# Performance work log

Hardware: AMD Instinct MI355X
Metric: run time of the kernel (lower is better)

Reference implementation:

```python
import jax, jax.numpy as jnp
import numpy as np


def causal_fft_conv(v, h):
    # v: [B, L, D], h: [L, D]; causal (linear, not circular) conv via zero-padded FFT
    L = v.shape[1]
    n = 2 * L
    Vf = jnp.fft.rfft(v, n=n, axis=1)          # [B, n//2+1, D]
    Hf = jnp.fft.rfft(h, n=n, axis=0)          # [n//2+1, D]
    y = jnp.fft.irfft(Vf * Hf[None], n=n, axis=1)
    return y[:, :L].astype(v.dtype)


def setup_inputs() -> dict:
    key = jax.random.key(0)
    ks = jax.random.split(key, 5)
    B, L, D = 4, 4096, 1024
    scale = 1.0 / np.sqrt(D)
    x = jax.random.normal(ks[0], (B, L, D), dtype=jnp.float32)
    Wu = jax.random.normal(ks[1], (D, D), dtype=jnp.float32) * scale
    Wv = jax.random.normal(ks[2], (D, D), dtype=jnp.float32) * scale
    Wo = jax.random.normal(ks[3], (D, D), dtype=jnp.float32) * scale
    h_filter = jax.random.normal(ks[4], (L, D), dtype=jnp.float32) * 0.02
    bu = jnp.zeros((D,), jnp.float32)
    bv = jnp.zeros((D,), jnp.float32)
    bo = jnp.zeros((D,), jnp.float32)
    return {"x": x, "Wu": Wu, "bu": bu, "Wv": Wv, "bv": bv,
            "h_filter": h_filter, "Wo": Wo, "bo": bo}


def reference(x, Wu, bu, Wv, bv, h_filter, Wo, bo):
    L = x.shape[1]
    u = jnp.einsum('bld,de->ble', x, Wu) + bu
    v = jnp.einsum('bld,de->ble', x, Wv) + bv
    t = jnp.arange(L, dtype=x.dtype)
    decay = jnp.exp(-0.01 * t)[:, None]          # [L, 1]
    h = h_filter * decay                          # [L, D]
    v_conv = causal_fft_conv(v, h)                # [B, L, D]
    y = u * v_conv
    y = jnp.einsum('bld,de->ble', y, Wo) + bo
    return y
```

## Files before the change

kernel.cpp:

```cpp
#include <hip/hip_runtime.h>
#include <hip/hip_bf16.h>
#include <hip/hip_fp16.h>
#include <string.h>

typedef __hip_bfloat16 bf16;
typedef _Float16 f16;
typedef __attribute__((ext_vector_type(8))) short short8;
typedef __attribute__((ext_vector_type(4))) float floatx4;
typedef __attribute__((ext_vector_type(4))) unsigned int uintx4;

#define GLD16(gp, lp) __builtin_amdgcn_global_load_lds( \
    (__attribute__((address_space(1))) void*)(gp),      \
    (__attribute__((address_space(3))) void*)(lp), 16, 0, 0)

__device__ __forceinline__ unsigned short bf16_bits(float f) {
  bf16 h = (bf16)f;
  unsigned short s;
  memcpy(&s, &h, 2);
  return s;
}

__global__ __launch_bounds__(256)
void cvtx_k(const float* __restrict__ x, char* __restrict__ outbase,
            size_t bstride) {
  size_t e = ((size_t)blockIdx.x * 256 + threadIdx.x) * 8;
  int b = (int)(e >> 22);
  size_t i = e & 4194303;
  const floatx4* s = (const floatx4*)(x + e);
  floatx4 a0 = s[0], a1 = s[1];
  union { uintx4 u4; unsigned short us[8]; } w;
  w.us[0] = bf16_bits(a0.x); w.us[1] = bf16_bits(a0.y);
  w.us[2] = bf16_bits(a0.z); w.us[3] = bf16_bits(a0.w);
  w.us[4] = bf16_bits(a1.x); w.us[5] = bf16_bits(a1.y);
  w.us[6] = bf16_bits(a1.z); w.us[7] = bf16_bits(a1.w);
  *(uintx4*)((bf16*)(outbase + (size_t)b * bstride) + i) = w.u4;
}

__global__ __launch_bounds__(256)
void transpose_k(const float* __restrict__ W0, const float* __restrict__ W1,
                 const float* __restrict__ W2, bf16* __restrict__ T0,
                 bf16* __restrict__ T1, bf16* __restrict__ T2) {
  __shared__ bf16 t[64][66];
  const float* S = blockIdx.z == 0 ? W0 : (blockIdx.z == 1 ? W1 : W2);
  bf16* Dst      = blockIdx.z == 0 ? T0 : (blockIdx.z == 1 ? T1 : T2);
  const int tx = threadIdx.x & 63, ty = threadIdx.x >> 6;
  const int kb = blockIdx.y * 64, nb = blockIdx.x * 64;
#pragma unroll
  for (int rr = 0; rr < 16; ++rr) {
    int r = ty * 16 + rr;
    t[r][tx] = (bf16)S[(size_t)(kb + r) * 1024 + nb + tx];
  }
  __syncthreads();
#pragma unroll
  for (int rr = 0; rr < 16; ++rr) {
    int r = ty * 16 + rr;
    Dst[(size_t)(nb + r) * 1024 + kb + tx] = t[tx][r];
  }
}

__global__ __launch_bounds__(256)
void hprep_k(const float* __restrict__ hf, f16* __restrict__ hp) {
  int idx = blockIdx.x * 256 + threadIdx.x;
  int dblk = idx >> 14;
  int rem = idx & 16383;
  int k = rem >> 5, dd = rem & 31;
  int d = dblk * 32 + dd;
  float val = hf[(size_t)k * 1024 + d] * __expf(-0.01f * (float)k);
  hp[idx] = (f16)val;
}

__device__ __forceinline__
void gemm_body(const bf16* __restrict__ A, const bf16* __restrict__ Bt,
               const float* __restrict__ bias, void* __restrict__ Cout,
               int out_mode, int m0, int n0) {
  constexpr int K = 1024;
  __shared__ __align__(16) bf16 As[128 * 32];
  __shared__ __align__(16) bf16 Bs[128 * 32];
  const int tid = threadIdx.x;
  const int lane = tid & 63;
  const int wave = tid >> 6;
  const int wm = wave >> 1, wn = wave & 1;
  const int r = lane & 15, q = lane >> 4;

  floatx4 acc[4][4] = {};

  const int s0 = tid, s1 = 256 + tid;
  const bf16* gA0 = A + (size_t)(m0 + (s0 >> 2)) * K + (s0 & 3) * 8;
  const bf16* gA1 = A + (size_t)(m0 + (s1 >> 2)) * K + (s1 & 3) * 8;
  const bf16* gB0 = Bt + (size_t)(n0 + (s0 >> 2)) * K + (s0 & 3) * 8;
  const bf16* gB1 = Bt + (size_t)(n0 + (s1 >> 2)) * K + (s1 & 3) * 8;
  char* AsB = (char*)As + wave * 1024;
  char* BsB = (char*)Bs + wave * 1024;

  for (int k0 = 0; k0 < K; k0 += 32) {
    GLD16(gA0 + k0, AsB);
    GLD16(gA1 + k0, AsB + 4096);
    GLD16(gB0 + k0, BsB);
    GLD16(gB1 + k0, BsB + 4096);
    __syncthreads();
    short8 af[4], bfr[4];
#pragma unroll
    for (int i = 0; i < 4; ++i)
      af[i] = *(const short8*)&As[(wm * 64 + i * 16 + r) * 32 + q * 8];
#pragma unroll
    for (int i = 0; i < 4; ++i)
      bfr[i] = *(const short8*)&Bs[(wn * 64 + i * 16 + r) * 32 + q * 8];
#pragma unroll
    for (int mi = 0; mi < 4; ++mi)
#pragma unroll
      for (int ni = 0; ni < 4; ++ni)
        acc[mi][ni] = __builtin_amdgcn_mfma_f32_16x16x32_bf16(
            af[mi], bfr[ni], acc[mi][ni], 0, 0, 0);
    __syncthreads();
  }

  const int cb = n0 + wn * 64;
  float bvv[4];
#pragma unroll
  for (int ni = 0; ni < 4; ++ni) bvv[ni] = bias[cb + ni * 16 + r];
#pragma unroll
  for (int mi = 0; mi < 4; ++mi) {
    int rowb = m0 + wm * 64 + mi * 16 + q * 4;
#pragma unroll
    for (int ni = 0; ni < 4; ++ni) {
      int col = cb + ni * 16 + r;
#pragma unroll
      for (int v = 0; v < 4; ++v) {
        float val = acc[mi][ni][v] + bvv[ni];
        size_t off = (size_t)(rowb + v) * 1024 + col;
        if (out_mode == 0)      ((bf16*)Cout)[off] = (bf16)val;
        else if (out_mode == 1) ((f16*)Cout)[off] = (f16)val;
        else                    ((float*)Cout)[off] = val;
      }
    }
  }
}

__global__ __launch_bounds__(256)
void gemm_uv_k(const bf16* __restrict__ A, const bf16* __restrict__ WuT,
               const bf16* __restrict__ WvT, const float* __restrict__ bu,
               const float* __restrict__ bv, bf16* __restrict__ u_out,
               f16* __restrict__ v_out) {
  const int isv = blockIdx.z;
  gemm_body(A, isv ? WvT : WuT, isv ? bv : bu,
            isv ? (void*)v_out : (void*)u_out, isv,
            blockIdx.x * 128, blockIdx.y * 128);
}

__global__ __launch_bounds__(256)
void gemm_o_k(const bf16* __restrict__ A, const bf16* __restrict__ Bt,
              const float* __restrict__ bias, float* __restrict__ C) {
  gemm_body(A, Bt, bias, (void*)C, 2, blockIdx.x * 128, blockIdx.y * 128);
}

__global__ __launch_bounds__(256)
void conv_k(const f16* __restrict__ vg0, const f16* __restrict__ hp,
            bf16* __restrict__ up0) {
  constexpr int KC = 128, D = 1024;
  __shared__ __align__(16) f16 hs[KC * 32];
  __shared__ __align__(16) f16 vs[256 * 32];
  const int tid = threadIdx.x;
  const int dd = tid & 31, tg = tid >> 5;
  const int d0 = blockIdx.x * 32;
  const int t0 = blockIdx.y * 128;
  const int base = tg * 16;
  const f16* vg = vg0 + (size_t)blockIdx.z * 4096 * D;
  bf16* up = up0 + (size_t)blockIdx.z * 4096 * D;

  float acc[16];
#pragma unroll
  for (int i = 0; i < 16; ++i) acc[i] = 0.f;

  const unsigned* vg32 = (const unsigned*)vg;
  unsigned* vs32 = (unsigned*)vs;
  const uintx4* hsrc = (const uintx4*)(hp + (size_t)blockIdx.x * 512 * 32);
  uintx4* hdst = (uintx4*)hs;

  for (int c = 0; c < 4; ++c) {
    const int k0 = c * KC;
    __syncthreads();
    hdst[tid] = hsrc[k0 * 4 + tid];
    hdst[tid + 256] = hsrc[k0 * 4 + tid + 256];
#pragma unroll
    for (int it = 0; it < 16; ++it) {
      int w = it * 256 + tid;
      int to = w >> 4, dp = w & 15;
      int tau = t0 - k0 - 128 + to;
      unsigned val = 0;
      if (tau >= 0) val = vg32[(size_t)tau * (D / 2) + (d0 >> 1) + dp];
      vs32[w] = val;
    }
    __syncthreads();
    float p[16];
#pragma unroll
    for (int i = 0; i < 16; ++i)
      p[i] = (float)vs[(base + i + 128) * 32 + dd];
    for (int kb = 0; kb < KC / 16; ++kb) {
#pragma unroll
      for (int k2 = 0; k2 < 16; ++k2) {
        const int kk = kb * 16 + k2;
        float hk = (float)hs[kk * 32 + dd];
#pragma unroll
        for (int i = 0; i < 16; ++i)
          acc[i] += hk * p[(i - k2) & 15];
        p[(15 - k2) & 15] = (float)vs[(base + 127 - kk) * 32 + dd];
      }
    }
  }

  const size_t rb = (size_t)(t0 + base) * D + d0 + dd;
#pragma unroll
  for (int i = 0; i < 16; ++i) {
    float uv = (float)up[rb + (size_t)i * D];
    up[rb + (size_t)i * D] = (bf16)(uv * acc[i]);
  }
}

extern "C" void kernel_launch(void* const* d_in, const int* in_sizes, int n_in,
                              void* d_out, int out_size, void* d_ws,
                              size_t ws_size, hipStream_t stream) {
  const float* x  = (const float*)d_in[0];
  const float* Wu = (const float*)d_in[1];
  const float* bu = (const float*)d_in[2];
  const float* Wv = (const float*)d_in[3];
  const float* bv = (const float*)d_in[4];
  const float* hf = (const float*)d_in[5];
  const float* Wo = (const float*)d_in[6];
  const float* bo = (const float*)d_in[7];
  char* ws = (char*)d_ws;
  bf16* WuT = (bf16*)(ws);
  bf16* WvT = (bf16*)(ws + 2097152);
  bf16* WoT = (bf16*)(ws + 4194304);
  f16*  hp  = (f16*)(ws + 6291456);

  dim3 tb(256);
  transpose_k<<<dim3(16, 16, 3), tb, 0, stream>>>(Wu, Wv, Wo, WuT, WvT, WoT);
  hprep_k<<<dim3(2048), tb, 0, stream>>>(hf, hp);

  if (ws_size >= 42991616ull) {
    bf16* xb = (bf16*)d_out;
    f16*  vf = (f16*)((char*)d_out + 33554432);
    bf16* u  = (bf16*)(ws + 8388608);
    cvtx_k<<<dim3(8192), tb, 0, stream>>>(x, (char*)d_out, 8388608);
    gemm_uv_k<<<dim3(128, 8, 2), tb, 0, stream>>>(xb, WuT, WvT, bu, bv, u, vf);
    conv_k<<<dim3(32, 32, 4), tb, 0, stream>>>(vf, hp, u);
    gemm_o_k<<<dim3(128, 8), tb, 0, stream>>>(u, WoT, bo, (float*)d_out);
  } else {
    bf16* u_b = (bf16*)(ws + 8388608);
    cvtx_k<<<dim3(8192), tb, 0, stream>>>(x, (char*)d_out, 16777216);
    for (int b = 0; b < 4; ++b) {
      char* quarter = (char*)d_out + (size_t)b * 16777216;
      bf16* xb = (bf16*)quarter;
      f16*  vb = (f16*)(quarter + 8388608);
      float* outb = (float*)d_out + (size_t)b * 4194304;
      gemm_uv_k<<<dim3(32, 8, 2), tb, 0, stream>>>(xb, WuT, WvT, bu, bv,
                                                   u_b, vb);
      conv_k<<<dim3(32, 32, 1), tb, 0, stream>>>(vb, hp, u_b);
      gemm_o_k<<<dim3(32, 8), tb, 0, stream>>>(u_b, WoT, bo, outb);
    }
  }
}
```

Before: 516.3 us.

## Use packed half2 FMA in causal conv with per-chunk fp16 accumulation

The direct-convolution kernel now has each thread process two adjacent channels as __half2, using packed __hfma2 instead of scalar fp32 FMAs. Partial sums accumulate in fp16 over each 64-tap chunk and are then folded into fp32 accumulators. Tiles now cover 64 channels with 128-bit loads, the filter prep layout changes to match, and the u-gating epilogue works on packed bf16 pairs. This targets ALU throughput in the convolution, at the cost of lower accumulation precision.

```diff
diff --git a/kernel.cpp b/kernel.cpp
--- a/kernel.cpp
+++ b/kernel.cpp
@@ -18,6 +18,11 @@
   unsigned short s;
   memcpy(&s, &h, 2);
   return s;
+}
+__device__ __forceinline__ __half2 u2h2(unsigned u) {
+  __half2 h;
+  memcpy(&h, &u, 4);
+  return h;
 }
 
 __global__ __launch_bounds__(256)
@@ -61,10 +66,10 @@
 __global__ __launch_bounds__(256)
 void hprep_k(const float* __restrict__ hf, f16* __restrict__ hp) {
   int idx = blockIdx.x * 256 + threadIdx.x;
-  int dblk = idx >> 14;
-  int rem = idx & 16383;
-  int k = rem >> 5, dd = rem & 31;
-  int d = dblk * 32 + dd;
+  int dblk = idx >> 15;
+  int rem = idx & 32767;
+  int k = rem >> 6, dd = rem & 63;
+  int d = dblk * 64 + dd;
   float val = hf[(size_t)k * 1024 + d] * __expf(-0.01f * (float)k);
   hp[idx] = (f16)val;
 }
@@ -156,63 +161,81 @@
 __global__ __launch_bounds__(256)
 void conv_k(const f16* __restrict__ vg0, const f16* __restrict__ hp,
             bf16* __restrict__ up0) {
-  constexpr int KC = 128, D = 1024;
-  __shared__ __align__(16) f16 hs[KC * 32];
-  __shared__ __align__(16) f16 vs[256 * 32];
+  constexpr int CC = 64, TT = 128, D = 1024;
+  __shared__ __align__(16) unsigned vs2[(TT + CC) * 32];
+  __shared__ __align__(16) unsigned hs2[CC * 32];
   const int tid = threadIdx.x;
-  const int dd = tid & 31, tg = tid >> 5;
-  const int d0 = blockIdx.x * 32;
-  const int t0 = blockIdx.y * 128;
+  const int pp = tid & 31, tg = tid >> 5;
+  const int bx = blockIdx.x;
+  const int t0 = blockIdx.y * TT;
   const int base = tg * 16;
-  const f16* vg = vg0 + (size_t)blockIdx.z * 4096 * D;
-  bf16* up = up0 + (size_t)blockIdx.z * 4096 * D;
-
-  float acc[16];
-#pragma unroll
-  for (int i = 0; i < 16; ++i) acc[i] = 0.f;
-
-  const unsigned* vg32 = (const unsigned*)vg;
-  unsigned* vs32 = (unsigned*)vs;
-  const uintx4* hsrc = (const uintx4*)(hp + (size_t)blockIdx.x * 512 * 32);
-  uintx4* hdst = (uintx4*)hs;
-
-  for (int c = 0; c < 4; ++c) {
-    const int k0 = c * KC;
-    __syncthreads();
-    hdst[tid] = hsrc[k0 * 4 + tid];
-    hdst[tid + 256] = hsrc[k0 * 4 + tid + 256];
-#pragma unroll
-    for (int it = 0; it < 16; ++it) {
-      int w = it * 256 + tid;
-      int to = w >> 4, dp = w & 15;
-      int tau = t0 - k0 - 128 + to;
-      unsigned val = 0;
-      if (tau >= 0) val = vg32[(size_t)tau * (D / 2) + (d0 >> 1) + dp];
-      vs32[w] = val;
-    }
-    __syncthreads();
-    float p[16];
+  const unsigned* vg32 = (const unsigned*)(vg0 + (size_t)blockIdx.z * 4096 * D);
+  unsigned* up32 = (unsigned*)(up0 + (size_t)blockIdx.z * 4096 * D);
+  const uintx4* vg4 = (const uintx4*)vg32;
+  const uintx4* hp4 = (const uintx4*)hp + (size_t)bx * 512 * 8;
+
+  float ax[16], ay[16];
+#pragma unroll
+  for (int i = 0; i < 16; ++i) { ax[i] = 0.f; ay[i] = 0.f; }
+
+  for (int c = 0; c < 8; ++c) {
+    const int k0 = c * CC;
+    __syncthreads();
+    {
+      uintx4* hd = (uintx4*)hs2;
+      hd[tid] = hp4[k0 * 8 + tid];
+      hd[tid + 256] = hp4[k0 * 8 + tid + 256];
+    }
+    {
+      uintx4* vd = (uintx4*)vs2;
+#pragma unroll
+      for (int it = 0; it < 6; ++it) {
+        int q = it * 256 + tid;
+        int row = q >> 3, dp4 = q & 7;
+        int tau = t0 - k0 - CC + row;
+        uintx4 val = {0, 0, 0, 0};
+        if (tau >= 0) val = vg4[(size_t)tau * 128 + bx * 8 + dp4];
+        vd[q] = val;
+      }
+    }
+    __syncthreads();
+
+    __half2 p[16];
 #pragma unroll
     for (int i = 0; i < 16; ++i)
-      p[i] = (float)vs[(base + i + 128) * 32 + dd];
-    for (int kb = 0; kb < KC / 16; ++kb) {
+      p[i] = u2h2(vs2[(base + i + CC) * 32 + pp]);
+    __half2 acc2[16];
+    const __half2 z2 = __float2half2_rn(0.f);
+#pragma unroll
+    for (int i = 0; i < 16; ++i) acc2[i] = z2;
+
+    for (int kb = 0; kb < 4; ++kb) {
 #pragma unroll
       for (int k2 = 0; k2 < 16; ++k2) {
         const int kk = kb * 16 + k2;
-        float hk = (float)hs[kk * 32 + dd];
+        __half2 hk = u2h2(hs2[kk * 32 + pp]);
 #pragma unroll
         for (int i = 0; i < 16; ++i)
-          acc[i] += hk * p[(i - k2) & 15];
-        p[(15 - k2) & 15] = (float)vs[(base + 127 - kk) * 32 + dd];
+          acc2[i] = __hfma2(hk, p[(i - k2) & 15], acc2[i]);
+        p[(15 - k2) & 15] = u2h2(vs2[(base + CC - 1 - kk) * 32 + pp]);
       }
     }
-  }
-
-  const size_t rb = (size_t)(t0 + base) * D + d0 + dd;
+#pragma unroll
+    for (int i = 0; i < 16; ++i) {
+      ax[i] += __low2float(acc2[i]);
+      ay[i] += __high2float(acc2[i]);
+    }
+  }
+
+  const size_t rb = (size_t)(t0 + base) * 512 + bx * 32 + pp;
 #pragma unroll
   for (int i = 0; i < 16; ++i) {
-    float uv = (float)up[rb + (size_t)i * D];
-    up[rb + (size_t)i * D] = (bf16)(uv * acc[i]);
+    unsigned uw = up32[rb + (size_t)i * 512];
+    float ul = __uint_as_float((uw & 0xffffu) << 16);
+    float uh = __uint_as_float(uw & 0xffff0000u);
+    unsigned lo = bf16_bits(ul * ax[i]);
+    unsigned hi = bf16_bits(uh * ay[i]);
+    up32[rb + (size_t)i * 512] = lo | (hi << 16);
   }
 }
 
@@ -243,7 +266,7 @@
     bf16* u  = (bf16*)(ws + 8388608);
     cvtx_k<<<dim3(8192), tb, 0, stream>>>(x, (char*)d_out, 8388608);
     gemm_uv_k<<<dim3(128, 8, 2), tb, 0, stream>>>(xb, WuT, WvT, bu, bv, u, vf);
-    conv_k<<<dim3(32, 32, 4), tb, 0, stream>>>(vf, hp, u);
+    conv_k<<<dim3(16, 32, 4), tb, 0, stream>>>(vf, hp, u);
     gemm_o_k<<<dim3(128, 8), tb, 0, stream>>>(u, WoT, bo, (float*)d_out);
   } else {
     bf16* u_b = (bf16*)(ws + 8388608);
@@ -255,7 +278,7 @@
       float* outb = (float*)d_out + (size_t)b * 4194304;
       gemm_uv_k<<<dim3(32, 8, 2), tb, 0, stream>>>(xb, WuT, WvT, bu, bv,
                                                    u_b, vb);
-      conv_k<<<dim3(32, 32, 1), tb, 0, stream>>>(vb, hp, u_b);
+      conv_k<<<dim3(16, 32, 1), tb, 0, stream>>>(vb, hp, u_b);
       gemm_o_k<<<dim3(32, 8), tb, 0, stream>>>(u_b, WoT, bo, outb);
     }
   }
```

Measured after the change: 436.4 us. -15.5%, faster.
